# Optimization experiments

Hardware: AMD Instinct MI355X
Metric: run time of the kernel (lower is better)

The kernel has to match this reference:

```python
import jax, jax.numpy as jnp
import numpy as np

B, LQ, LK = 2, 2048, 2048
QDIM, KDIM, VDIM, HID, H = 1024, 768, 768, 1024, 16
D = HID // H  # head_dim = 64


def setup_inputs() -> dict:
    key = jax.random.key(0)
    ks = jax.random.split(key, 12)
    s = 0.02
    return {
        "query": jax.random.normal(ks[0], (B, LQ, QDIM), jnp.float32),
        "key": jax.random.normal(ks[1], (B, LK, KDIM), jnp.float32),
        "value": jax.random.normal(ks[2], (B, LK, VDIM), jnp.float32),
        "Wq": jax.random.normal(ks[3], (QDIM, HID), jnp.float32) * s,
        "bq": jnp.zeros((HID,), jnp.float32),
        "Wk": jax.random.normal(ks[4], (KDIM, HID), jnp.float32) * s,
        "bk": jnp.zeros((HID,), jnp.float32),
        "Wv": jax.random.normal(ks[5], (VDIM, HID), jnp.float32) * s,
        "bv": jnp.zeros((HID,), jnp.float32),
        "Wo": jax.random.normal(ks[6], (HID, QDIM), jnp.float32) * s,
        "bo": jnp.zeros((QDIM,), jnp.float32),
        "query_mask": jax.random.randint(ks[7], (B, LQ), 0, 2, jnp.int32),
        "key_mask": jnp.ones((B, LK), jnp.int32),
    }


def reference(query, key, value, Wq, bq, Wk, bk, Wv, bv, Wo, bo, query_mask, key_mask):
    # projections -> [B, L, H, D] -> [B, H, L, D]
    q = (query @ Wq + bq).reshape(B, LQ, H, D).transpose(0, 2, 1, 3)
    k = (key @ Wk + bk).reshape(B, LK, H, D).transpose(0, 2, 1, 3)
    v = (value @ Wv + bv).reshape(B, LK, H, D).transpose(0, 2, 1, 3)

    scores = jnp.einsum("bhqd,bhkd->bhqk", q, k) / jnp.sqrt(jnp.asarray(D, q.dtype))
    # Faithful to the torch code: query_mask masks the LAST (key) axis,
    # key_mask masks the QUERY axis (requires LQ == LK).
    neg_inf = jnp.asarray(-jnp.inf, scores.dtype)
    scores = jnp.where(query_mask[:, None, None, :] == 0, neg_inf, scores)
    scores = jnp.where(key_mask[:, None, :, None] == 0, neg_inf, scores)

    attn = jax.nn.softmax(scores, axis=-1)  # dropout is identity in eval / p=0
    ctx = jnp.einsum("bhqk,bhkd->bqhd", attn, v).reshape(B, LQ, HID)
    return ctx @ Wo + bo
```

## Files before the change

kernel.cpp:

```cpp
#include <hip/hip_runtime.h>
#include <hip/hip_bf16.h>

#define B_   2
#define LQ_  2048
#define LK_  2048
#define QDIM_ 1024
#define KDIM_ 768
#define VDIM_ 768
#define HID_ 1024
#define H_   16
#define D_   64

typedef unsigned short ushort_t;
typedef __attribute__((ext_vector_type(8))) short short8v;
typedef __attribute__((ext_vector_type(4))) float f32x4;

__device__ __forceinline__ float bf2f(unsigned short u) {
    union { unsigned int i; float f; } x; x.i = ((unsigned int)u) << 16; return x.f;
}
__device__ __forceinline__ unsigned short f2bf(float f) {
    union { float f; unsigned int i; } x; x.f = f;
    unsigned int r = x.i + 0x7FFFu + ((x.i >> 16) & 1u);
    return (unsigned short)(r >> 16);
}
__device__ __forceinline__ float exp2_(float x) {
#if defined(__has_builtin) && __has_builtin(__builtin_amdgcn_exp2f)
    return __builtin_amdgcn_exp2f(x);
#else
    return __expf(x * 0.69314718055994531f);
#endif
}
__device__ __forceinline__ unsigned cvtpk_bf16(float lo, float hi) {
    unsigned r;
    asm("v_cvt_pk_bf16_f32 %0, %1, %2" : "=v"(r) : "v"(lo), "v"(hi));
    return r;
}
__device__ __forceinline__ unsigned perm_b32(unsigned hi, unsigned lo, unsigned sel) {
#if defined(__has_builtin) && __has_builtin(__builtin_amdgcn_perm)
    return __builtin_amdgcn_perm(hi, lo, sel);
#else
    unsigned r = 0;
    for (int i = 0; i < 4; ++i) {
        unsigned s = (sel >> (8 * i)) & 0xFF;
        unsigned byte = (s < 4) ? ((lo >> (8 * s)) & 0xFF) : ((hi >> (8 * (s - 4))) & 0xFF);
        r |= byte << (8 * i);
    }
    return r;
#endif
}
__device__ __forceinline__ void stage16(const ushort_t* g, ushort_t* l) {
#if defined(__has_builtin) && __has_builtin(__builtin_amdgcn_global_load_lds)
    __builtin_amdgcn_global_load_lds(
        (const __attribute__((address_space(1))) unsigned*)g,
        (__attribute__((address_space(3))) unsigned*)l, 16, 0, 0);
#else
    *(uint4*)l = *(const uint4*)g;
#endif
}

__global__ void detect_dtype(const ushort_t* __restrict__ q, int* __restrict__ flag) {
    const int tid = threadIdx.x;
    float m = 0.f;
    for (int i = tid; i < 4096; i += 64) m = fmaxf(m, fabsf(bf2f(q[i])));
    #pragma unroll
    for (int off = 1; off < 64; off <<= 1) m = fmaxf(m, __shfl_xor(m, off));
    if (tid == 0) flag[0] = (m < 1000.0f) ? 1 : 0;
}

__global__ __launch_bounds__(256) void transpose_any(
    const void* __restrict__ in, ushort_t* __restrict__ out,
    int R, int C, const int* __restrict__ flagp)
{
    __shared__ ushort_t tile[32][33];
    const int isbf = flagp[0];
    const int tx = threadIdx.x & 31;
    const int ty = threadIdx.x >> 5;
    const int r0 = blockIdx.y * 32, c0 = blockIdx.x * 32;
    #pragma unroll
    for (int j = 0; j < 4; ++j) {
        int r = r0 + ty + j * 8;
        ushort_t v;
        if (isbf) v = ((const ushort_t*)in)[(size_t)r * C + c0 + tx];
        else      v = f2bf(((const float*)in)[(size_t)r * C + c0 + tx]);
        tile[ty + j * 8][tx] = v;
    }
    __syncthreads();
    #pragma unroll
    for (int j = 0; j < 4; ++j) {
        int c = c0 + ty + j * 8;
        out[(size_t)c * R + r0 + tx] = tile[tx][ty + j * 8];
    }
}

__device__ __forceinline__ void gemm_core(
    const void* __restrict__ A, const ushort_t* __restrict__ WT,
    const void* __restrict__ bias, void* __restrict__ Cp,
    int M, int N, int K, int isbf, int a_bf, int c_bf, float out_scale,
    int wg, ushort_t (*As)[128][32], ushort_t (*Bs)[128][32])
{
    const int tid = threadIdx.x;
    const int l = tid & 63, w = tid >> 6;
    const int g = l >> 4, q = l & 15;
    const int wr = (w >> 1) * 64, wc = (w & 1) * 64;
    const int nbn = N >> 7;
    const int bm = (wg / nbn) * 128;
    const int bn = (wg % nbn) * 128;

    const int r_ = tid >> 2;
    const int c_ = tid & 3;
    const int sc_ = ((c_ ^ (r_ & 3)) << 3);
    const int dc_ = c_ << 3;

    f32x4 acc[4][4];
    #pragma unroll
    for (int i = 0; i < 4; ++i)
        #pragma unroll
        for (int j = 0; j < 4; ++j)
            acc[i][j] = (f32x4){0.f, 0.f, 0.f, 0.f};

    const int NT = K >> 5;
    float4 fA[4];

    auto issue = [&](int t, int buf) {
        const int koff = t << 5;
        if (a_bf) {
            stage16((const ushort_t*)A + (size_t)(bm + r_) * K + koff + sc_,
                    &As[buf][r_][dc_]);
            stage16((const ushort_t*)A + (size_t)(bm + 64 + r_) * K + koff + sc_,
                    &As[buf][64 + r_][dc_]);
        } else {
            const float* Af0 = (const float*)A + (size_t)(bm + r_) * K + koff + dc_;
            const float* Af1 = (const float*)A + (size_t)(bm + 64 + r_) * K + koff + dc_;
            fA[0] = *(const float4*)Af0; fA[1] = *(const float4*)(Af0 + 4);
            fA[2] = *(const float4*)Af1; fA[3] = *(const float4*)(Af1 + 4);
        }
        stage16(WT + (size_t)(bn + r_) * K + koff + sc_, &Bs[buf][r_][dc_]);
        stage16(WT + (size_t)(bn + 64 + r_) * K + koff + sc_, &Bs[buf][64 + r_][dc_]);
    };
    auto commitA = [&](int buf) {
        ushort_t t0[8], t1[8];
        t0[0]=f2bf(fA[0].x); t0[1]=f2bf(fA[0].y); t0[2]=f2bf(fA[0].z); t0[3]=f2bf(fA[0].w);
        t0[4]=f2bf(fA[1].x); t0[5]=f2bf(fA[1].y); t0[6]=f2bf(fA[1].z); t0[7]=f2bf(fA[1].w);
        t1[0]=f2bf(fA[2].x); t1[1]=f2bf(fA[2].y); t1[2]=f2bf(fA[2].z); t1[3]=f2bf(fA[2].w);
        t1[4]=f2bf(fA[3].x); t1[5]=f2bf(fA[3].y); t1[6]=f2bf(fA[3].z); t1[7]=f2bf(fA[3].w);
        *(uint4*)&As[buf][r_][sc_]      = *(uint4*)t0;
        *(uint4*)&As[buf][64 + r_][sc_] = *(uint4*)t1;
    };

    issue(0, 0);
    if (!a_bf) commitA(0);
    __syncthreads();

    int cur = 0;
    const int fcol = ((g ^ (q & 3)) << 3);
    for (int t = 0; t < NT; ++t) {
        const bool has = (t + 1 < NT);
        if (has) issue(t + 1, cur ^ 1);

        short8v a[4], bb[4];
        #pragma unroll
        for (int mf = 0; mf < 4; ++mf)
            a[mf] = *(const short8v*)&As[cur][wr + mf * 16 + q][fcol];
        #pragma unroll
        for (int nf = 0; nf < 4; ++nf)
            bb[nf] = *(const short8v*)&Bs[cur][wc + nf * 16 + q][fcol];
        #pragma unroll
        for (int mf = 0; mf < 4; ++mf)
            #pragma unroll
            for (int nf = 0; nf < 4; ++nf)
                acc[mf][nf] = __builtin_amdgcn_mfma_f32_16x16x32_bf16(a[mf], bb[nf], acc[mf][nf], 0, 0, 0);

        if (has && !a_bf) commitA(cur ^ 1);
        __syncthreads();
        cur ^= 1;
    }

    float bv[4];
    #pragma unroll
    for (int nf = 0; nf < 4; ++nf) {
        int col = bn + wc + nf * 16 + q;
        bv[nf] = isbf ? bf2f(((const ushort_t*)bias)[col]) : ((const float*)bias)[col];
    }
    #pragma unroll
    for (int mf = 0; mf < 4; ++mf)
        #pragma unroll
        for (int nf = 0; nf < 4; ++nf)
            #pragma unroll
            for (int reg = 0; reg < 4; ++reg) {
                int row = bm + wr + mf * 16 + g * 4 + reg;
                int col = bn + wc + nf * 16 + q;
                float vv = (acc[mf][nf][reg] + bv[nf]) * out_scale;
                if (c_bf) ((ushort_t*)Cp)[(size_t)row * N + col] = f2bf(vv);
                else      ((float*)Cp)[(size_t)row * N + col] = vv;
            }
}

struct G3 {
    const void* A0; const void* A1; const void* A2;
    const ushort_t* W0; const ushort_t* W1; const ushort_t* W2;
    const void* b0; const void* b1; const void* b2;
    void* C0; void* C1; void* C2;
    int K0, K1, K2;
    float s0, s1, s2;
};

__global__ __launch_bounds__(256) void gemm3_mfma(G3 p, int M, int N,
                                                  const int* __restrict__ flagp)
{
    __shared__ ushort_t As[2][128][32];
    __shared__ ushort_t Bs[2][128][32];
    const int isbf = flagp[0];
    const int op = blockIdx.y;
    const void* A = (op == 0) ? p.A0 : (op == 1) ? p.A1 : p.A2;
    const ushort_t* WT = (op == 0) ? p.W0 : (op == 1) ? p.W1 : p.W2;
    const void* bias = (op == 0) ? p.b0 : (op == 1) ? p.b1 : p.b2;
    void* C = (op == 0) ? p.C0 : (op == 1) ? p.C1 : p.C2;
    const int K = (op == 0) ? p.K0 : (op == 1) ? p.K1 : p.K2;
    const float sc = (op == 0) ? p.s0 : (op == 1) ? p.s1 : p.s2;
    const int cpx = gridDim.x >> 3;
    const int wg = (blockIdx.x & 7) * cpx + (blockIdx.x >> 3);
    gemm_core(A, WT, bias, C, M, N, K, isbf, isbf , 1 , sc, wg, As, Bs);
}

__global__ __launch_bounds__(256) void gemm_one(
    const void* __restrict__ A, const ushort_t* __restrict__ WT,
    const void* __restrict__ bias, void* __restrict__ Cp,
    int M, int N, int K, const int* __restrict__ flagp, float out_scale)
{
    __shared__ ushort_t As[2][128][32];
    __shared__ ushort_t Bs[2][128][32];
    const int isbf = flagp[0];
    const int cpx = gridDim.x >> 3;
    const int wg = (blockIdx.x & 7) * cpx + (blockIdx.x >> 3);
    gemm_core(A, WT, bias, Cp, M, N, K, isbf, 1, isbf, out_scale, wg, As, Bs);
}

__global__ __launch_bounds__(512, 4) void attn_mfma(
    const ushort_t* __restrict__ Q, const ushort_t* __restrict__ Kp,
    const ushort_t* __restrict__ Vp, const int* __restrict__ qmask,
    const int* __restrict__ kmask, ushort_t* __restrict__ ctx)
{
    __shared__ ushort_t sQ[128][64];
    __shared__ ushort_t sK[2][64][64];
    __shared__ ushort_t sVt[2][64][64];
    __shared__ ushort_t sP[8][16][64];
    __shared__ unsigned sMaskPk[2][32];

    const int tid = threadIdx.x;
    const int l = tid & 63, w = tid >> 6;
    const int g = l >> 4, q = l & 15;
    const int b = blockIdx.z, h = blockIdx.y;
    const int q0 = blockIdx.x * 128;
    const size_t hoff = (size_t)h * 64;
    const int swz = (q & 7) << 3;

    const int vp = tid & 255;
    const int vk2 = (vp & 31) * 2;
    const int vdb = vp >> 5;
    const int vds = (tid >> 8) * 4;

    const int krow = tid >> 3, ks = tid & 7;
    const int kscol = ((ks ^ (krow & 7)) << 3);

    #pragma unroll
    for (int i = 0; i < 2; ++i) {
        int chunk = tid + 512 * i;
        int row = chunk >> 3, s = chunk & 7;
        stage16(Q + ((size_t)(b * LQ_) + q0 + row) * HID_ + hoff + ((s ^ (row & 7)) << 3),
                &sQ[row][s << 3]);
    }
    stage16(Kp + ((size_t)(b * LK_) + krow) * HID_ + hoff + kscol, &sK[0][krow][ks << 3]);
    {
        size_t basev = ((size_t)(b * LK_) + vk2) * HID_ + hoff + vdb * 8 + vds;
        uint2 va = *(const uint2*)(Vp + basev);
        uint2 vb2 = *(const uint2*)(Vp + basev + HID_);
        #pragma unroll
        for (int t2 = 0; t2 < 2; ++t2) {
            unsigned d0w = ((const unsigned*)&va)[t2], d1w = ((const unsigned*)&vb2)[t2];
            unsigned lo = perm_b32(d1w, d0w, 0x05040100);
            unsigned hi = perm_b32(d1w, d0w, 0x07060302);
            int dr0 = vdb * 8 + vds + 2 * t2, dr1 = dr0 + 1;
            *(unsigned*)&sVt[0][dr0][vk2 ^ ((dr0 & 7) << 3)] = lo;
            *(unsigned*)&sVt[0][dr1][vk2 ^ ((dr1 & 7) << 3)] = hi;
        }
    }
    if (w == 0) {
        unsigned long long bits = __ballot(qmask[b * LQ_ + l] != 0);
        if (l < 32) {
            unsigned dw = (((bits >> (2 * l)) & 1ull) ? 0xFFFFu : 0u)
                        | (((bits >> (2 * l + 1)) & 1ull) ? 0xFFFF0000u : 0u);
            sMaskPk[0][l] = dw;
        }
    }
    __syncthreads();

    const int myq = 16 * w + q;
    short8v qf[2];
    qf[0] = *(const short8v*)&sQ[myq][(g << 3) ^ swz];
    qf[1] = *(const short8v*)&sQ[myq][(32 + (g << 3)) ^ swz];
    const int rowm = kmask[b * LK_ + q0 + myq];

    short8v ones;
    #pragma unroll
    for (int j = 0; j < 8; ++j) ones[j] = (short)0x3F80;

    float m_run = -1e30f;
    f32x4 o[4], o4;
    #pragma unroll
    for (int df = 0; df < 4; ++df) o[df] = (f32x4){0.f, 0.f, 0.f, 0.f};
    o4 = (f32x4){0.f, 0.f, 0.f, 0.f};

    int cur = 0;
    for (int t0 = 0; t0 < LK_; t0 += 64) {
        const int t0n = t0 + 64;
        const bool has = (t0n < LK_);
        uint2 va, vb2;
        if (has) {
            size_t basev = ((size_t)(b * LK_) + t0n + vk2) * HID_ + hoff + vdb * 8 + vds;
            va = *(const uint2*)(Vp + basev);
            vb2 = *(const uint2*)(Vp + basev + HID_);
            stage16(Kp + ((size_t)(b * LK_) + t0n + krow) * HID_ + hoff + kscol,
                    &sK[cur ^ 1][krow][ks << 3]);
            if (w == 0) {
                unsigned long long bits = __ballot(qmask[b * LQ_ + t0n + l] != 0);
                if (l < 32) {
                    unsigned dw = (((bits >> (2 * l)) & 1ull) ? 0xFFFFu : 0u)
                                | (((bits >> (2 * l + 1)) & 1ull) ? 0xFFFF0000u : 0u);
                    sMaskPk[cur ^ 1][l] = dw;
                }
            }
        }

        f32x4 s4[4];
        #pragma unroll
        for (int kf = 0; kf < 4; ++kf) s4[kf] = (f32x4){0.f, 0.f, 0.f, 0.f};
        #pragma unroll
        for (int kf = 0; kf < 4; ++kf) {
            short8v k0f = *(const short8v*)&sK[cur][kf * 16 + q][(g << 3) ^ swz];
            short8v k1f = *(const short8v*)&sK[cur][kf * 16 + q][(32 + (g << 3)) ^ swz];
            s4[kf] = __builtin_amdgcn_mfma_f32_16x16x32_bf16(k0f, qf[0], s4[kf], 0, 0, 0);
            s4[kf] = __builtin_amdgcn_mfma_f32_16x16x32_bf16(k1f, qf[1], s4[kf], 0, 0, 0);
        }

        float tmx[8];
        #pragma unroll
        for (int i = 0; i < 8; ++i) tmx[i] = fmaxf(s4[i >> 2][i & 3], s4[2 + (i >> 2)][i & 3]);
        #pragma unroll
        for (int st = 4; st >= 1; st >>= 1)
            #pragma unroll
            for (int i = 0; i < st; ++i) tmx[i] = fmaxf(tmx[i], tmx[i + st]);
        float lm = tmx[0];
        lm = fmaxf(lm, __shfl_xor(lm, 16));
        lm = fmaxf(lm, __shfl_xor(lm, 32));

        const bool fullp = __any(lm - m_run > 8.0f) != 0;
        float mnew, corr;
        if (fullp) { mnew = fmaxf(m_run, lm); corr = exp2_(m_run - mnew); }
        else       { mnew = m_run;            corr = 1.0f; }

        float pf[16];
        #pragma unroll
        for (int kf = 0; kf < 4; ++kf)
            #pragma unroll
            for (int reg = 0; reg < 4; ++reg)
                pf[kf * 4 + reg] = exp2_(s4[kf][reg] - mnew);
        m_run = mnew;

        #pragma unroll
        for (int kf = 0; kf < 4; ++kf) {
            uint2 pv;
            pv.x = cvtpk_bf16(pf[kf * 4 + 0], pf[kf * 4 + 1]);
            pv.y = cvtpk_bf16(pf[kf * 4 + 2], pf[kf * 4 + 3]);
            *(uint2*)&sP[w][q][(kf * 16 + g * 4) ^ swz] = pv;
        }

        if (fullp) {
            #pragma unroll
            for (int df = 0; df < 4; ++df)
                #pragma unroll
                for (int reg = 0; reg < 4; ++reg) o[df][reg] *= corr;
            #pragma unroll
            for (int reg = 0; reg < 4; ++reg) o4[reg] *= corr;
        }

        #pragma unroll
        for (int s2 = 0; s2 < 2; ++s2) {
            uint4 paw = *(const uint4*)&sP[w][q][((s2 * 32) + (g << 3)) ^ swz];
            uint4 mk = *(const uint4*)&sMaskPk[cur][s2 * 16 + g * 4];
            paw.x &= mk.x; paw.y &= mk.y; paw.z &= mk.z; paw.w &= mk.w;
            short8v pa;
            __builtin_memcpy(&pa, &paw, 16);
            #pragma unroll
            for (int df = 0; df < 4; ++df) {
                short8v vb = *(const short8v*)&sVt[cur][df * 16 + q][((s2 * 32) + (g << 3)) ^ swz];
                o[df] = __builtin_amdgcn_mfma_f32_16x16x32_bf16(vb, pa, o[df], 0, 0, 0);
            }
            o4 = __builtin_amdgcn_mfma_f32_16x16x32_bf16(ones, pa, o4, 0, 0, 0);
        }

        if (has) {
            #pragma unroll
            for (int t2 = 0; t2 < 2; ++t2) {
                unsigned d0w = ((const unsigned*)&va)[t2], d1w = ((const unsigned*)&vb2)[t2];
                unsigned lo = perm_b32(d1w, d0w, 0x05040100);
                unsigned hi = perm_b32(d1w, d0w, 0x07060302);
                int dr0 = vdb * 8 + vds + 2 * t2, dr1 = dr0 + 1;
                *(unsigned*)&sVt[cur ^ 1][dr0][vk2 ^ ((dr0 & 7) << 3)] = lo;
                *(unsigned*)&sVt[cur ^ 1][dr1][vk2 ^ ((dr1 & 7) << 3)] = hi;
            }
        }
        __syncthreads();
        cur ^= 1;
    }

    const float lr = o4[0];
    const float lq = (rowm != 0 && lr > 0.f) ? (1.f / lr) : 0.f;
    const size_t obase = ((size_t)(b * LQ_) + q0 + myq) * HID_ + hoff;
    #pragma unroll
    for (int df = 0; df < 4; ++df) {
        uint2 st;
        st.x = cvtpk_bf16(o[df][0] * lq, o[df][1] * lq);
        st.y = cvtpk_bf16(o[df][2] * lq, o[df][3] * lq);
        *(uint2*)&ctx[obase + df * 16 + g * 4] = st;
    }
}

extern "C" void kernel_launch(void* const* d_in, const int* in_sizes, int n_in,
                              void* d_out, int out_size, void* d_ws, size_t ws_size,
                              hipStream_t stream) {
    const int* qmask = (const int*)d_in[11];
    const int* kmask = (const int*)d_in[12];

    const size_t M = (size_t)B_ * LQ_;
    int* flag = (int*)d_ws;
    ushort_t* qx = (ushort_t*)((char*)d_ws + 256);
    ushort_t* kx = qx + M * HID_;
    ushort_t* vx = kx + M * HID_;
    ushort_t* cx = vx + M * HID_;
    ushort_t* WTq = cx;
    ushort_t* WTk = WTq + 1024 * 1024;
    ushort_t* WTv = WTk + 1024 * 768;
    ushort_t* WTo = qx;

    const float QSCALE = 0.125f * 1.4426950408889634f;

    detect_dtype<<<1, 64, 0, stream>>>((const ushort_t*)d_in[0], flag);

    transpose_any<<<dim3(HID_ / 32, QDIM_ / 32), 256, 0, stream>>>(d_in[3], WTq, QDIM_, HID_, flag);
    transpose_any<<<dim3(HID_ / 32, KDIM_ / 32), 256, 0, stream>>>(d_in[5], WTk, KDIM_, HID_, flag);
    transpose_any<<<dim3(HID_ / 32, VDIM_ / 32), 256, 0, stream>>>(d_in[7], WTv, VDIM_, HID_, flag);

    G3 p;
    p.A0 = d_in[0]; p.A1 = d_in[1]; p.A2 = d_in[2];
    p.W0 = WTq;     p.W1 = WTk;     p.W2 = WTv;
    p.b0 = d_in[4]; p.b1 = d_in[6]; p.b2 = d_in[8];
    p.C0 = qx;      p.C1 = kx;      p.C2 = vx;
    p.K0 = QDIM_;   p.K1 = KDIM_;   p.K2 = VDIM_;
    p.s0 = QSCALE;  p.s1 = 1.0f;    p.s2 = 1.0f;
    const int nwg = (int)(M / 128) * (HID_ / 128);
    gemm3_mfma<<<dim3(nwg, 3), 256, 0, stream>>>(p, (int)M, HID_, flag);

    attn_mfma<<<dim3(LQ_ / 128, H_, B_), 512, 0, stream>>>(qx, kx, vx, qmask, kmask, cx);

    transpose_any<<<dim3(QDIM_ / 32, HID_ / 32), 256, 0, stream>>>(d_in[9], WTo, HID_, QDIM_, flag);
    gemm_one<<<dim3((int)(M / 128) * (QDIM_ / 128)), 256, 0, stream>>>(
        cx, WTo, d_in[10], d_out, (int)M, QDIM_, HID_, flag, 1.0f);
}
```

Baseline: 158.5 us.

## Merge weight transposes, narrow output GEMM tile, pipeline attention V loads deeper

Combines the four weight transposes into one launch. The output projection GEMM uses a 128x64 tile so more workgroups can run. Attention drops the shared-memory Q staging in favour of direct register loads, prefetches V two tiles ahead with a manually unrolled ping-pong, and raises the occupancy hint. Attention output is written in place over the Q buffer to free workspace for the transposed output weight. The higher occupancy hint may add register pressure or spills, and the smaller GEMM tile reduces data reuse.

```diff
diff --git a/kernel.cpp b/kernel.cpp
--- a/kernel.cpp
+++ b/kernel.cpp
@@ -67,15 +67,24 @@
     if (tid == 0) flag[0] = (m < 1000.0f) ? 1 : 0;
 }
 
-__global__ __launch_bounds__(256) void transpose_any(
-    const void* __restrict__ in, ushort_t* __restrict__ out,
-    int R, int C, const int* __restrict__ flagp)
+__global__ __launch_bounds__(256) void transpose4(
+    const void* __restrict__ W0, const void* __restrict__ W1,
+    const void* __restrict__ W2, const void* __restrict__ W3,
+    ushort_t* __restrict__ O0, ushort_t* __restrict__ O1,
+    ushort_t* __restrict__ O2, ushort_t* __restrict__ O3,
+    const int* __restrict__ flagp)
 {
     __shared__ ushort_t tile[32][33];
     const int isbf = flagp[0];
+    const int op = blockIdx.z;
+    const void* in = (op == 0) ? W0 : (op == 1) ? W1 : (op == 2) ? W2 : W3;
+    ushort_t* out  = (op == 0) ? O0 : (op == 1) ? O1 : (op == 2) ? O2 : O3;
+    const int R = (op == 1 || op == 2) ? KDIM_ : 1024;
+    const int C = 1024;
     const int tx = threadIdx.x & 31;
     const int ty = threadIdx.x >> 5;
     const int r0 = blockIdx.y * 32, c0 = blockIdx.x * 32;
+    if (r0 >= R) return;
     #pragma unroll
     for (int j = 0; j < 4; ++j) {
         int r = r0 + ty + j * 8;
@@ -92,30 +101,32 @@
     }
 }
 
+template<int TBN>
 __device__ __forceinline__ void gemm_core(
     const void* __restrict__ A, const ushort_t* __restrict__ WT,
     const void* __restrict__ bias, void* __restrict__ Cp,
     int M, int N, int K, int isbf, int a_bf, int c_bf, float out_scale,
-    int wg, ushort_t (*As)[128][32], ushort_t (*Bs)[128][32])
+    int wg, ushort_t (*As)[32], ushort_t (*Bs)[32])
 {
+    constexpr int NF = TBN / 32;
     const int tid = threadIdx.x;
     const int l = tid & 63, w = tid >> 6;
     const int g = l >> 4, q = l & 15;
-    const int wr = (w >> 1) * 64, wc = (w & 1) * 64;
-    const int nbn = N >> 7;
+    const int wr = (w >> 1) * 64, wc = (w & 1) * (TBN / 2);
+    const int nbn = N / TBN;
     const int bm = (wg / nbn) * 128;
-    const int bn = (wg % nbn) * 128;
+    const int bn = (wg % nbn) * TBN;
 
     const int r_ = tid >> 2;
     const int c_ = tid & 3;
     const int sc_ = ((c_ ^ (r_ & 3)) << 3);
     const int dc_ = c_ << 3;
 
-    f32x4 acc[4][4];
+    f32x4 acc[4][NF];
     #pragma unroll
     for (int i = 0; i < 4; ++i)
         #pragma unroll
-        for (int j = 0; j < 4; ++j)
+        for (int j = 0; j < NF; ++j)
             acc[i][j] = (f32x4){0.f, 0.f, 0.f, 0.f};
 
     const int NT = K >> 5;
@@ -125,17 +136,18 @@
         const int koff = t << 5;
         if (a_bf) {
             stage16((const ushort_t*)A + (size_t)(bm + r_) * K + koff + sc_,
-                    &As[buf][r_][dc_]);
+                    &As[(buf << 7) + r_][dc_]);
             stage16((const ushort_t*)A + (size_t)(bm + 64 + r_) * K + koff + sc_,
-                    &As[buf][64 + r_][dc_]);
+                    &As[(buf << 7) + 64 + r_][dc_]);
         } else {
             const float* Af0 = (const float*)A + (size_t)(bm + r_) * K + koff + dc_;
             const float* Af1 = (const float*)A + (size_t)(bm + 64 + r_) * K + koff + dc_;
             fA[0] = *(const float4*)Af0; fA[1] = *(const float4*)(Af0 + 4);
             fA[2] = *(const float4*)Af1; fA[3] = *(const float4*)(Af1 + 4);
         }
-        stage16(WT + (size_t)(bn + r_) * K + koff + sc_, &Bs[buf][r_][dc_]);
-        stage16(WT + (size_t)(bn + 64 + r_) * K + koff + sc_, &Bs[buf][64 + r_][dc_]);
+        stage16(WT + (size_t)(bn + r_) * K + koff + sc_, &Bs[buf * TBN + r_][dc_]);
+        if (TBN == 128)
+            stage16(WT + (size_t)(bn + 64 + r_) * K + koff + sc_, &Bs[buf * TBN + 64 + r_][dc_]);
     };
     auto commitA = [&](int buf) {
         ushort_t t0[8], t1[8];
@@ -143,8 +155,8 @@
         t0[4]=f2bf(fA[1].x); t0[5]=f2bf(fA[1].y); t0[6]=f2bf(fA[1].z); t0[7]=f2bf(fA[1].w);
         t1[0]=f2bf(fA[2].x); t1[1]=f2bf(fA[2].y); t1[2]=f2bf(fA[2].z); t1[3]=f2bf(fA[2].w);
         t1[4]=f2bf(fA[3].x); t1[5]=f2bf(fA[3].y); t1[6]=f2bf(fA[3].z); t1[7]=f2bf(fA[3].w);
-        *(uint4*)&As[buf][r_][sc_]      = *(uint4*)t0;
-        *(uint4*)&As[buf][64 + r_][sc_] = *(uint4*)t1;
+        *(uint4*)&As[(buf << 7) + r_][sc_]      = *(uint4*)t0;
+        *(uint4*)&As[(buf << 7) + 64 + r_][sc_] = *(uint4*)t1;
     };
 
     issue(0, 0);
@@ -157,17 +169,17 @@
         const bool has = (t + 1 < NT);
         if (has) issue(t + 1, cur ^ 1);
 
-        short8v a[4], bb[4];
+        short8v a[4], bb[NF];
         #pragma unroll
         for (int mf = 0; mf < 4; ++mf)
-            a[mf] = *(const short8v*)&As[cur][wr + mf * 16 + q][fcol];
-        #pragma unroll
-        for (int nf = 0; nf < 4; ++nf)
-            bb[nf] = *(const short8v*)&Bs[cur][wc + nf * 16 + q][fcol];
+            a[mf] = *(const short8v*)&As[(cur << 7) + wr + mf * 16 + q][fcol];
+        #pragma unroll
+        for (int nf = 0; nf < NF; ++nf)
+            bb[nf] = *(const short8v*)&Bs[cur * TBN + wc + nf * 16 + q][fcol];
         #pragma unroll
         for (int mf = 0; mf < 4; ++mf)
             #pragma unroll
-            for (int nf = 0; nf < 4; ++nf)
+            for (int nf = 0; nf < NF; ++nf)
                 acc[mf][nf] = __builtin_amdgcn_mfma_f32_16x16x32_bf16(a[mf], bb[nf], acc[mf][nf], 0, 0, 0);
 
         if (has && !a_bf) commitA(cur ^ 1);
@@ -175,16 +187,16 @@
         cur ^= 1;
     }
 
-    float bv[4];
-    #pragma unroll
-    for (int nf = 0; nf < 4; ++nf) {
+    float bv[NF];
+    #pragma unroll
+    for (int nf = 0; nf < NF; ++nf) {
         int col = bn + wc + nf * 16 + q;
         bv[nf] = isbf ? bf2f(((const ushort_t*)bias)[col]) : ((const float*)bias)[col];
     }
     #pragma unroll
     for (int mf = 0; mf < 4; ++mf)
         #pragma unroll
-        for (int nf = 0; nf < 4; ++nf)
+        for (int nf = 0; nf < NF; ++nf)
             #pragma unroll
             for (int reg = 0; reg < 4; ++reg) {
                 int row = bm + wr + mf * 16 + g * 4 + reg;
@@ -207,8 +219,8 @@
 __global__ __launch_bounds__(256) void gemm3_mfma(G3 p, int M, int N,
                                                   const int* __restrict__ flagp)
 {
-    __shared__ ushort_t As[2][128][32];
-    __shared__ ushort_t Bs[2][128][32];
+    __shared__ ushort_t As[2 * 128][32];
+    __shared__ ushort_t Bs[2 * 128][32];
     const int isbf = flagp[0];
     const int op = blockIdx.y;
     const void* A = (op == 0) ? p.A0 : (op == 1) ? p.A1 : p.A2;
@@ -219,7 +231,7 @@
     const float sc = (op == 0) ? p.s0 : (op == 1) ? p.s1 : p.s2;
     const int cpx = gridDim.x >> 3;
     const int wg = (blockIdx.x & 7) * cpx + (blockIdx.x >> 3);
-    gemm_core(A, WT, bias, C, M, N, K, isbf, isbf , 1 , sc, wg, As, Bs);
+    gemm_core<128>(A, WT, bias, C, M, N, K, isbf, isbf, 1, sc, wg, As, Bs);
 }
 
 __global__ __launch_bounds__(256) void gemm_one(
@@ -227,20 +239,19 @@
     const void* __restrict__ bias, void* __restrict__ Cp,
     int M, int N, int K, const int* __restrict__ flagp, float out_scale)
 {
-    __shared__ ushort_t As[2][128][32];
-    __shared__ ushort_t Bs[2][128][32];
+    __shared__ ushort_t As[2 * 128][32];
+    __shared__ ushort_t Bs[2 * 64][32];
     const int isbf = flagp[0];
     const int cpx = gridDim.x >> 3;
     const int wg = (blockIdx.x & 7) * cpx + (blockIdx.x >> 3);
-    gemm_core(A, WT, bias, Cp, M, N, K, isbf, 1, isbf, out_scale, wg, As, Bs);
-}
-
-__global__ __launch_bounds__(512, 4) void attn_mfma(
+    gemm_core<64>(A, WT, bias, Cp, M, N, K, isbf, 1, isbf, out_scale, wg, As, Bs);
+}
+
+__global__ __launch_bounds__(512, 6) void attn_mfma(
     const ushort_t* __restrict__ Q, const ushort_t* __restrict__ Kp,
     const ushort_t* __restrict__ Vp, const int* __restrict__ qmask,
     const int* __restrict__ kmask, ushort_t* __restrict__ ctx)
 {
-    __shared__ ushort_t sQ[128][64];
     __shared__ ushort_t sK[2][64][64];
     __shared__ ushort_t sVt[2][64][64];
     __shared__ ushort_t sP[8][16][64];
@@ -254,51 +265,63 @@
     const size_t hoff = (size_t)h * 64;
     const int swz = (q & 7) << 3;
 
-    const int vp = tid & 255;
-    const int vk2 = (vp & 31) * 2;
-    const int vdb = vp >> 5;
+    const int vpi = tid & 255;
+    const int vk2 = (vpi & 31) * 2;
+    const int vdb = vpi >> 5;
     const int vds = (tid >> 8) * 4;
+    const size_t vbase0 = ((size_t)(b * LK_) + vk2) * HID_ + hoff + vdb * 8 + vds;
 
     const int krow = tid >> 3, ks = tid & 7;
     const int kscol = ((ks ^ (krow & 7)) << 3);
-
-    #pragma unroll
-    for (int i = 0; i < 2; ++i) {
-        int chunk = tid + 512 * i;
-        int row = chunk >> 3, s = chunk & 7;
-        stage16(Q + ((size_t)(b * LQ_) + q0 + row) * HID_ + hoff + ((s ^ (row & 7)) << 3),
-                &sQ[row][s << 3]);
-    }
-    stage16(Kp + ((size_t)(b * LK_) + krow) * HID_ + hoff + kscol, &sK[0][krow][ks << 3]);
-    {
-        size_t basev = ((size_t)(b * LK_) + vk2) * HID_ + hoff + vdb * 8 + vds;
-        uint2 va = *(const uint2*)(Vp + basev);
-        uint2 vb2 = *(const uint2*)(Vp + basev + HID_);
+    const size_t kbase0 = ((size_t)(b * LK_) + krow) * HID_ + hoff + kscol;
+
+    const int myq = 16 * w + q;
+    const ushort_t* Qrow = Q + ((size_t)(b * LQ_) + q0 + myq) * HID_ + hoff;
+    short8v qf0 = *(const short8v*)(Qrow + g * 8);
+    short8v qf1 = *(const short8v*)(Qrow + 32 + g * 8);
+    const int rowm = kmask[b * LK_ + q0 + myq];
+
+    auto loadV = [&](int t, uint2& a, uint2& c) {
+        size_t base = vbase0 + (size_t)t * 64 * HID_;
+        a = *(const uint2*)(Vp + base);
+        c = *(const uint2*)(Vp + base + HID_);
+    };
+    auto writeV = [&](int buf, uint2 a, uint2 c) {
         #pragma unroll
         for (int t2 = 0; t2 < 2; ++t2) {
-            unsigned d0w = ((const unsigned*)&va)[t2], d1w = ((const unsigned*)&vb2)[t2];
+            unsigned d0w = t2 ? a.y : a.x;
+            unsigned d1w = t2 ? c.y : c.x;
             unsigned lo = perm_b32(d1w, d0w, 0x05040100);
             unsigned hi = perm_b32(d1w, d0w, 0x07060302);
             int dr0 = vdb * 8 + vds + 2 * t2, dr1 = dr0 + 1;
-            *(unsigned*)&sVt[0][dr0][vk2 ^ ((dr0 & 7) << 3)] = lo;
-            *(unsigned*)&sVt[0][dr1][vk2 ^ ((dr1 & 7) << 3)] = hi;
-        }
-    }
-    if (w == 0) {
-        unsigned long long bits = __ballot(qmask[b * LQ_ + l] != 0);
-        if (l < 32) {
-            unsigned dw = (((bits >> (2 * l)) & 1ull) ? 0xFFFFu : 0u)
-                        | (((bits >> (2 * l + 1)) & 1ull) ? 0xFFFF0000u : 0u);
-            sMaskPk[0][l] = dw;
-        }
-    }
+            *(unsigned*)&sVt[buf][dr0][vk2 ^ ((dr0 & 7) << 3)] = lo;
+            *(unsigned*)&sVt[buf][dr1][vk2 ^ ((dr1 & 7) << 3)] = hi;
+        }
+    };
+    auto stageK = [&](int t, int buf) {
+        stage16(Kp + kbase0 + (size_t)t * 64 * HID_, &sK[buf][krow][ks << 3]);
+    };
+    auto stageMask = [&](int t, int buf) {
+        if (w == 0) {
+            unsigned long long bits = __ballot(qmask[b * LQ_ + t * 64 + l] != 0);
+            if (l < 32) {
+                unsigned dw = (((bits >> (2 * l)) & 1ull) ? 0xFFFFu : 0u)
+                            | (((bits >> (2 * l + 1)) & 1ull) ? 0xFFFF0000u : 0u);
+                sMaskPk[buf][l] = dw;
+            }
+        }
+    };
+
+    uint2 vA0, vA1, vB0, vB1;
+    {
+        uint2 a, c;
+        loadV(0, a, c);
+        writeV(0, a, c);
+    }
+    stageK(0, 0);
+    stageMask(0, 0);
+    loadV(1, vA0, vA1);
     __syncthreads();
-
-    const int myq = 16 * w + q;
-    short8v qf[2];
-    qf[0] = *(const short8v*)&sQ[myq][(g << 3) ^ swz];
-    qf[1] = *(const short8v*)&sQ[myq][(32 + (g << 3)) ^ swz];
-    const int rowm = kmask[b * LK_ + q0 + myq];
 
     short8v ones;
     #pragma unroll
@@ -310,36 +333,21 @@
     for (int df = 0; df < 4; ++df) o[df] = (f32x4){0.f, 0.f, 0.f, 0.f};
     o4 = (f32x4){0.f, 0.f, 0.f, 0.f};
 
-    int cur = 0;
-    for (int t0 = 0; t0 < LK_; t0 += 64) {
-        const int t0n = t0 + 64;
-        const bool has = (t0n < LK_);
-        uint2 va, vb2;
-        if (has) {
-            size_t basev = ((size_t)(b * LK_) + t0n + vk2) * HID_ + hoff + vdb * 8 + vds;
-            va = *(const uint2*)(Vp + basev);
-            vb2 = *(const uint2*)(Vp + basev + HID_);
-            stage16(Kp + ((size_t)(b * LK_) + t0n + krow) * HID_ + hoff + kscol,
-                    &sK[cur ^ 1][krow][ks << 3]);
-            if (w == 0) {
-                unsigned long long bits = __ballot(qmask[b * LQ_ + t0n + l] != 0);
-                if (l < 32) {
-                    unsigned dw = (((bits >> (2 * l)) & 1ull) ? 0xFFFFu : 0u)
-                                | (((bits >> (2 * l + 1)) & 1ull) ? 0xFFFF0000u : 0u);
-                    sMaskPk[cur ^ 1][l] = dw;
-                }
-            }
-        }
+    auto step = [&](int t, int curb, uint2& wv0, uint2& wv1, uint2& iv0, uint2& iv1) {
+        const bool hasW = (t + 1 < 32);
+        const bool hasI = (t + 2 < 32);
+        if (hasI) loadV(t + 2, iv0, iv1);
+        if (hasW) { stageK(t + 1, curb ^ 1); stageMask(t + 1, curb ^ 1); }
 
         f32x4 s4[4];
         #pragma unroll
         for (int kf = 0; kf < 4; ++kf) s4[kf] = (f32x4){0.f, 0.f, 0.f, 0.f};
         #pragma unroll
         for (int kf = 0; kf < 4; ++kf) {
-            short8v k0f = *(const short8v*)&sK[cur][kf * 16 + q][(g << 3) ^ swz];
-            short8v k1f = *(const short8v*)&sK[cur][kf * 16 + q][(32 + (g << 3)) ^ swz];
-            s4[kf] = __builtin_amdgcn_mfma_f32_16x16x32_bf16(k0f, qf[0], s4[kf], 0, 0, 0);
-            s4[kf] = __builtin_amdgcn_mfma_f32_16x16x32_bf16(k1f, qf[1], s4[kf], 0, 0, 0);
+            short8v k0f = *(const short8v*)&sK[curb][kf * 16 + q][(g << 3) ^ swz];
+            short8v k1f = *(const short8v*)&sK[curb][kf * 16 + q][(32 + (g << 3)) ^ swz];
+            s4[kf] = __builtin_amdgcn_mfma_f32_16x16x32_bf16(k0f, qf0, s4[kf], 0, 0, 0);
+            s4[kf] = __builtin_amdgcn_mfma_f32_16x16x32_bf16(k1f, qf1, s4[kf], 0, 0, 0);
         }
 
         float tmx[8];
@@ -358,19 +366,18 @@
         if (fullp) { mnew = fmaxf(m_run, lm); corr = exp2_(m_run - mnew); }
         else       { mnew = m_run;            corr = 1.0f; }
 
-        float pf[16];
         #pragma unroll
         for (int kf = 0; kf < 4; ++kf)
             #pragma unroll
             for (int reg = 0; reg < 4; ++reg)
-                pf[kf * 4 + reg] = exp2_(s4[kf][reg] - mnew);
+                s4[kf][reg] = exp2_(s4[kf][reg] - mnew);
         m_run = mnew;
 
         #pragma unroll
         for (int kf = 0; kf < 4; ++kf) {
             uint2 pv;
-            pv.x = cvtpk_bf16(pf[kf * 4 + 0], pf[kf * 4 + 1]);
-            pv.y = cvtpk_bf16(pf[kf * 4 + 2], pf[kf * 4 + 3]);
+            pv.x = cvtpk_bf16(s4[kf][0], s4[kf][1]);
+            pv.y = cvtpk_bf16(s4[kf][2], s4[kf][3]);
             *(uint2*)&sP[w][q][(kf * 16 + g * 4) ^ swz] = pv;
         }
 
@@ -386,42 +393,36 @@
         #pragma unroll
         for (int s2 = 0; s2 < 2; ++s2) {
             uint4 paw = *(const uint4*)&sP[w][q][((s2 * 32) + (g << 3)) ^ swz];
-            uint4 mk = *(const uint4*)&sMaskPk[cur][s2 * 16 + g * 4];
+            uint4 mk = *(const uint4*)&sMaskPk[curb][s2 * 16 + g * 4];
             paw.x &= mk.x; paw.y &= mk.y; paw.z &= mk.z; paw.w &= mk.w;
             short8v pa;
             __builtin_memcpy(&pa, &paw, 16);
             #pragma unroll
             for (int df = 0; df < 4; ++df) {
-                short8v vb = *(const short8v*)&sVt[cur][df * 16 + q][((s2 * 32) + (g << 3)) ^ swz];
+                short8v vb = *(const short8v*)&sVt[curb][df * 16 + q][((s2 * 32) + (g << 3)) ^ swz];
                 o[df] = __builtin_amdgcn_mfma_f32_16x16x32_bf16(vb, pa, o[df], 0, 0, 0);
             }
             o4 = __builtin_amdgcn_mfma_f32_16x16x32_bf16(ones, pa, o4, 0, 0, 0);
         }
 
-        if (has) {
-            #pragma unroll
-            for (int t2 = 0; t2 < 2; ++t2) {
-                unsigned d0w = ((const unsigned*)&va)[t2], d1w = ((const unsigned*)&vb2)[t2];
-                unsigned lo = perm_b32(d1w, d0w, 0x05040100);
-                unsigned hi = perm_b32(d1w, d0w, 0x07060302);
-                int dr0 = vdb * 8 + vds + 2 * t2, dr1 = dr0 + 1;
-                *(unsigned*)&sVt[cur ^ 1][dr0][vk2 ^ ((dr0 & 7) << 3)] = lo;
-                *(unsigned*)&sVt[cur ^ 1][dr1][vk2 ^ ((dr1 & 7) << 3)] = hi;
-            }
-        }
+        if (hasW) writeV(curb ^ 1, wv0, wv1);
         __syncthreads();
-        cur ^= 1;
+    };
+
+    for (int t2 = 0; t2 < 32; t2 += 2) {
+        step(t2,     0, vA0, vA1, vB0, vB1);
+        step(t2 + 1, 1, vB0, vB1, vA0, vA1);
     }
 
     const float lr = o4[0];
-    const float lq = (rowm != 0 && lr > 0.f) ? (1.f / lr) : 0.f;
-    const size_t obase = ((size_t)(b * LQ_) + q0 + myq) * HID_ + hoff;
+    const float lqv = (rowm != 0 && lr > 0.f) ? (1.f / lr) : 0.f;
+    ushort_t* orow = ctx + ((size_t)(b * LQ_) + q0 + myq) * HID_ + hoff;
     #pragma unroll
     for (int df = 0; df < 4; ++df) {
         uint2 st;
-        st.x = cvtpk_bf16(o[df][0] * lq, o[df][1] * lq);
-        st.y = cvtpk_bf16(o[df][2] * lq, o[df][3] * lq);
-        *(uint2*)&ctx[obase + df * 16 + g * 4] = st;
+        st.x = cvtpk_bf16(o[df][0] * lqv, o[df][1] * lqv);
+        st.y = cvtpk_bf16(o[df][2] * lqv, o[df][3] * lqv);
+        *(uint2*)(orow + df * 16 + g * 4) = st;
     }
 }
 
@@ -440,15 +441,14 @@
     ushort_t* WTq = cx;
     ushort_t* WTk = WTq + 1024 * 1024;
     ushort_t* WTv = WTk + 1024 * 768;
-    ushort_t* WTo = qx;
+    ushort_t* WTo = WTv + 1024 * 768;
 
     const float QSCALE = 0.125f * 1.4426950408889634f;
 
     detect_dtype<<<1, 64, 0, stream>>>((const ushort_t*)d_in[0], flag);
 
-    transpose_any<<<dim3(HID_ / 32, QDIM_ / 32), 256, 0, stream>>>(d_in[3], WTq, QDIM_, HID_, flag);
-    transpose_any<<<dim3(HID_ / 32, KDIM_ / 32), 256, 0, stream>>>(d_in[5], WTk, KDIM_, HID_, flag);
-    transpose_any<<<dim3(HID_ / 32, VDIM_ / 32), 256, 0, stream>>>(d_in[7], WTv, VDIM_, HID_, flag);
+    transpose4<<<dim3(32, 32, 4), 256, 0, stream>>>(
+        d_in[3], d_in[5], d_in[7], d_in[9], WTq, WTk, WTv, WTo, flag);
 
     G3 p;
     p.A0 = d_in[0]; p.A1 = d_in[1]; p.A2 = d_in[2];
@@ -460,9 +460,8 @@
     const int nwg = (int)(M / 128) * (HID_ / 128);
     gemm3_mfma<<<dim3(nwg, 3), 256, 0, stream>>>(p, (int)M, HID_, flag);
 
-    attn_mfma<<<dim3(LQ_ / 128, H_, B_), 512, 0, stream>>>(qx, kx, vx, qmask, kmask, cx);
-
-    transpose_any<<<dim3(QDIM_ / 32, HID_ / 32), 256, 0, stream>>>(d_in[9], WTo, HID_, QDIM_, flag);
-    gemm_one<<<dim3((int)(M / 128) * (QDIM_ / 128)), 256, 0, stream>>>(
-        cx, WTo, d_in[10], d_out, (int)M, QDIM_, HID_, flag, 1.0f);
-}
+    attn_mfma<<<dim3(LQ_ / 128, H_, B_), 512, 0, stream>>>(qx, kx, vx, qmask, kmask, qx);
+
+    gemm_one<<<dim3((int)(M / 128) * (QDIM_ / 64)), 256, 0, stream>>>(
+        qx, WTo, d_in[10], d_out, (int)M, QDIM_, HID_, flag, 1.0f);
+}
```

Measured after the change: 192.7 us. 21.6% more time.
